# Performance work log

Measured on AMD Instinct MI355X. Metric: run time of the kernel, lower is better.

Reference implementation:

```python
import jax, jax.numpy as jnp
import numpy as np

B, S, F = 64, 1024, 768          # batch, seq = num_patch*patch_size**2, d_model
H, DH = 12, 64                    # heads, head dim = out_dim // d
P2 = 64                           # patch_size ** 2 = attended window length
SCALE = 8.0                       # norm_scale ** 0.5 = (out_dim // d) ** 0.5


def setup_inputs() -> dict:
    key = jax.random.key(0)
    ks = jax.random.split(key, 10)
    std = 0.02
    return {
        "x": jax.random.normal(ks[0], (B, S, F), dtype=jnp.float32),
        # per-head q/k/v projection weights stacked: [H, DH, F] (Linear: y = x @ W.T + b)
        "Wq": jax.random.normal(ks[1], (H, DH, F), dtype=jnp.float32) * std,
        "bq": jax.random.normal(ks[2], (H, DH), dtype=jnp.float32) * std,
        "Wk": jax.random.normal(ks[3], (H, DH, F), dtype=jnp.float32) * std,
        "bk": jax.random.normal(ks[4], (H, DH), dtype=jnp.float32) * std,
        "Wv": jax.random.normal(ks[5], (H, DH, F), dtype=jnp.float32) * std,
        "bv": jax.random.normal(ks[6], (H, DH), dtype=jnp.float32) * std,
        # MHA output projection (only W_MSA[0] is ever used in the stage1 path)
        "Wo": jax.random.normal(ks[7], (F, F), dtype=jnp.float32) * std,
        "bo": jax.random.normal(ks[8], (F,), dtype=jnp.float32) * std,
    }


def reference(x, Wq, bq, Wk, bk, Wv, bv, Wo, bo):
    # stage1 path of SBlock1: only the first window (P2 tokens) goes through
    # MultiHeadAttention (W_MSA[0]); remaining windows are passed through raw
    # and concatenated along the sequence dim.
    xw = x[:, :P2, :]                                    # [B, P2, F]
    q = jnp.einsum('bsf,hdf->bhsd', xw, Wq) + bq[None, :, None, :]
    k = jnp.einsum('bsf,hdf->bhsd', xw, Wk) + bk[None, :, None, :]
    v = jnp.einsum('bsf,hdf->bhsd', xw, Wv) + bv[None, :, None, :]
    scores = jnp.einsum('bhsd,bhtd->bhst', q, k) / SCALE
    attn = jax.nn.softmax(scores, axis=-1)
    o = jnp.einsum('bhst,bhtd->bhsd', attn, v)           # [B, H, P2, DH]
    # heads concatenated along feature dim in order 0..H-1
    o = o.transpose(0, 2, 1, 3).reshape(xw.shape[0], P2, H * DH)
    o = o @ Wo.T + bo                                    # output projection
    return jnp.concatenate([o, x[:, P2:, :]], axis=1)    # [B, S, F]
```

## Files before the change

### kernel.cpp

```cpp
#include <hip/hip_runtime.h>

#define B_   64
#define S_   1024
#define F_   768
#define H_   12
#define DH_  64
#define P2_  64
#define NQKV 2304

using bf16x8 = __attribute__((ext_vector_type(8))) short;
using f32x4  = __attribute__((ext_vector_type(4))) float;

__device__ __forceinline__ unsigned short f2bf(float f) {
    union { float f; unsigned u; } v;
    v.f = f;
    unsigned r = v.u + 0x7FFF + ((v.u >> 16) & 1);
    return (unsigned short)(r >> 16);
}

__device__ __forceinline__ void gll16(const unsigned short* g, unsigned char* l) {
    __builtin_amdgcn_global_load_lds(
        (const __attribute__((address_space(1))) unsigned int*)g,
        (__attribute__((address_space(3))) unsigned int*)l, 16, 0, 0);
}

__global__ __launch_bounds__(256) void prep_kernel(
        const float* __restrict__ x,
        const float* __restrict__ Wq, const float* __restrict__ Wk,
        const float* __restrict__ Wv, const float* __restrict__ Wo,
        const float* __restrict__ bq, const float* __restrict__ bk,
        const float* __restrict__ bv,
        unsigned short* __restrict__ xw, unsigned short* __restrict__ Wqkv,
        unsigned short* __restrict__ Wob, float* __restrict__ bqv) {
    const int NW = 786432;
    const int W4 = 147456;
    int i = blockIdx.x * 256 + threadIdx.x;
    if (i < NW) {
        int b = i / 12288, r = i - b * 12288;
        float4 v = reinterpret_cast<const float4*>(x)[b * 196608 + r];
        ushort4 h;
        h.x = f2bf(v.x); h.y = f2bf(v.y); h.z = f2bf(v.z); h.w = f2bf(v.w);
        reinterpret_cast<ushort4*>(xw)[i] = h;
    } else if (i < NW + 3 * W4) {
        int j = i - NW;
        int which = j / W4, local = j - which * W4;
        const float* src = (which == 0) ? Wq : (which == 1) ? Wk : Wv;
        float4 v = reinterpret_cast<const float4*>(src)[local];
        ushort4 h;
        h.x = f2bf(v.x); h.y = f2bf(v.y); h.z = f2bf(v.z); h.w = f2bf(v.w);
        reinterpret_cast<ushort4*>(Wqkv)[j] = h;
    } else if (i < NW + 4 * W4) {
        int local = i - NW - 3 * W4;
        float4 v = reinterpret_cast<const float4*>(Wo)[local];
        ushort4 h;
        h.x = f2bf(v.x); h.y = f2bf(v.y); h.z = f2bf(v.z); h.w = f2bf(v.w);
        reinterpret_cast<ushort4*>(Wob)[local] = h;
    } else if (i < NW + 4 * W4 + 576) {
        int j4 = i - NW - 4 * W4;
        int seg = j4 / 192, local = j4 - seg * 192;
        const float* src = (seg == 0) ? bq : (seg == 1) ? bk : bv;
        reinterpret_cast<float4*>(bqv)[j4] =
            reinterpret_cast<const float4*>(src)[local];
    }
}

template <int BM, int BN, int OUT_MODE>
__device__ __forceinline__ void gemm_body(
        int bx, int by,
        const unsigned short* __restrict__ A, const unsigned short* __restrict__ Bw,
        const float* __restrict__ bias, void* __restrict__ Cout) {
    constexpr int WC = (BN == 128) ? 2 : 1;
    constexpr int WR = 4 / WC;
    constexpr int MI = BM / WR / 16;
    constexpr int NJ = BN / WC / 16;
    constexpr int CA = BM / 32;
    constexpr int CB = BN / 32;
    __shared__ __align__(16) unsigned char lds[(BM + BN) * 128];
    unsigned char* As = lds;
    unsigned char* Bs = lds + BM * 128;
    const int tid  = threadIdx.x;
    const int lane = tid & 63;
    const int w    = tid >> 6;
    const int wr = w / WC, wc = w % WC;
    const int mbase = wr * (BM / WR), nbase = wc * (BN / WC);
    const int m0 = by * BM, n0 = bx * BN;
    const int lr = lane >> 3, lc = lane & 7;

    f32x4 acc[MI][NJ] = {};

    for (int kt = 0; kt < 768; kt += 64) {
        __syncthreads();
#pragma unroll
        for (int p = 0; p < CA; ++p) {
            int row = (w * CA + p) * 8 + lr;
            gll16(A + (size_t)(m0 + row) * 768 + kt + ((lc ^ (row & 7)) << 3),
                  As + (w * CA + p) * 1024);
        }
#pragma unroll
        for (int p = 0; p < CB; ++p) {
            int row = (w * CB + p) * 8 + lr;
            gll16(Bw + (size_t)(n0 + row) * 768 + kt + ((lc ^ (row & 7)) << 3),
                  Bs + (w * CB + p) * 1024);
        }
        __syncthreads();
#pragma unroll
        for (int kk = 0; kk < 2; ++kk) {
            const int g = kk * 4 + (lane >> 4);
            bf16x8 a[MI], b[NJ];
#pragma unroll
            for (int i = 0; i < MI; ++i) {
                int row = mbase + i * 16 + (lane & 15);
                a[i] = *reinterpret_cast<const bf16x8*>(As + row * 128 + ((g ^ (row & 7)) << 4));
            }
#pragma unroll
            for (int j = 0; j < NJ; ++j) {
                int row = nbase + j * 16 + (lane & 15);
                b[j] = *reinterpret_cast<const bf16x8*>(Bs + row * 128 + ((g ^ (row & 7)) << 4));
            }
#pragma unroll
            for (int i = 0; i < MI; ++i)
#pragma unroll
                for (int j = 0; j < NJ; ++j)
                    acc[i][j] = __builtin_amdgcn_mfma_f32_16x16x32_bf16(a[i], b[j], acc[i][j], 0, 0, 0);
        }
    }

    float bj[NJ];
#pragma unroll
    for (int j = 0; j < NJ; ++j) bj[j] = bias[n0 + nbase + j * 16 + (lane & 15)];

#pragma unroll
    for (int i = 0; i < MI; ++i) {
        int mrow = m0 + mbase + i * 16 + ((lane >> 4) << 2);
#pragma unroll
        for (int j = 0; j < NJ; ++j) {
            int n = n0 + nbase + j * 16 + (lane & 15);
#pragma unroll
            for (int r = 0; r < 4; ++r) {
                float v = acc[i][j][r] + bj[j];
                if constexpr (OUT_MODE == 0) {
                    reinterpret_cast<unsigned short*>(Cout)[(size_t)(mrow + r) * 2304 + n] = f2bf(v);
                } else {
                    int m = mrow + r;
                    reinterpret_cast<float*>(Cout)[(size_t)(m >> 6) * 786432 + (m & 63) * 768 + n] = v;
                }
            }
        }
    }
}

__global__ __launch_bounds__(256) void mega_kernel(
        const float* __restrict__ x, float* __restrict__ out,
        const unsigned short* __restrict__ xw, const unsigned short* __restrict__ Wqkv,
        const float* __restrict__ bqv, unsigned short* __restrict__ Y) {
    if (blockIdx.x < 2048) {
        const int total4 = 11796480;
        int stride = 2048 * 256;
        for (int i = blockIdx.x * 256 + threadIdx.x; i < total4; i += stride) {
            int b = i / 184320, r = i - b * 184320;
            int idx = b * 196608 + 12288 + r;
            reinterpret_cast<float4*>(out)[idx] =
                reinterpret_cast<const float4*>(x)[idx];
        }
    } else {
        int gid = blockIdx.x - 2048;
        gemm_body<128, 128, 0>(gid % 18, gid / 18, xw, Wqkv, bqv, (void*)Y);
    }
}

__global__ __launch_bounds__(256) void oproj_kernel(
        const unsigned short* __restrict__ Obuf, const unsigned short* __restrict__ Wob,
        const float* __restrict__ bo, float* __restrict__ out) {
    gemm_body<64, 64, 1>(blockIdx.x, blockIdx.y, Obuf, Wob, bo, (void*)out);
}

__global__ __launch_bounds__(256) void attn_kernel(
        const unsigned short* __restrict__ Y, unsigned short* __restrict__ O) {
    const int bh = blockIdx.x;
    const int b = bh / 12, h = bh % 12;
    __shared__ __align__(16) unsigned char lds[32768];
    unsigned char* Qs = lds;
    unsigned char* Ks = lds + 8192;
    unsigned char* Vt = lds + 16384;
    unsigned char* Ps = lds + 24576;
    const int tid = threadIdx.x, lane = tid & 63, w = tid >> 6;

    for (int c = tid; c < 512; c += 256) {
        int row = c >> 3, cc = c & 7;
        const unsigned short* src = Y + (size_t)(b * 64 + row) * NQKV + h * 64 + cc * 8;
        *reinterpret_cast<int4*>(Qs + row * 128 + ((cc ^ (row & 7)) << 4)) =
            *reinterpret_cast<const int4*>(src);
        *reinterpret_cast<int4*>(Ks + row * 128 + ((cc ^ (row & 7)) << 4)) =
            *reinterpret_cast<const int4*>(src + 768);
        int4 vv = *reinterpret_cast<const int4*>(src + 1536);
        const unsigned short* vs = reinterpret_cast<const unsigned short*>(&vv);
#pragma unroll
        for (int u = 0; u < 8; ++u) {
            int d = cc * 8 + u;
            *reinterpret_cast<unsigned short*>(
                Vt + d * 128 + (((row >> 3) ^ u) << 4) + ((row & 7) << 1)) = vs[u];
        }
    }
    __syncthreads();

    f32x4 accS[4] = {};
#pragma unroll
    for (int kk = 0; kk < 2; ++kk) {
        const int g = kk * 4 + (lane >> 4);
        int qrow = w * 16 + (lane & 15);
        bf16x8 a = *reinterpret_cast<const bf16x8*>(Qs + qrow * 128 + ((g ^ (qrow & 7)) << 4));
#pragma unroll
        for (int j = 0; j < 4; ++j) {
            int krow = j * 16 + (lane & 15);
            bf16x8 bb = *reinterpret_cast<const bf16x8*>(Ks + krow * 128 + ((g ^ (krow & 7)) << 4));
            accS[j] = __builtin_amdgcn_mfma_f32_16x16x32_bf16(a, bb, accS[j], 0, 0, 0);
        }
    }

#pragma unroll
    for (int r = 0; r < 4; ++r) {
        float v0 = accS[0][r], v1 = accS[1][r], v2 = accS[2][r], v3 = accS[3][r];
        float mx = fmaxf(fmaxf(v0, v1), fmaxf(v2, v3));
        mx = fmaxf(mx, __shfl_xor(mx, 1));
        mx = fmaxf(mx, __shfl_xor(mx, 2));
        mx = fmaxf(mx, __shfl_xor(mx, 4));
        mx = fmaxf(mx, __shfl_xor(mx, 8));
        float p0 = __expf((v0 - mx) * 0.125f);
        float p1 = __expf((v1 - mx) * 0.125f);
        float p2 = __expf((v2 - mx) * 0.125f);
        float p3 = __expf((v3 - mx) * 0.125f);
        float sm = p0 + p1 + p2 + p3;
        sm += __shfl_xor(sm, 1);
        sm += __shfl_xor(sm, 2);
        sm += __shfl_xor(sm, 4);
        sm += __shfl_xor(sm, 8);
        float inv = 1.0f / sm;
        int srow = w * 16 + ((lane >> 4) << 2) + r;
        float pv[4] = {p0 * inv, p1 * inv, p2 * inv, p3 * inv};
#pragma unroll
        for (int j = 0; j < 4; ++j) {
            int t = j * 16 + (lane & 15);
            *reinterpret_cast<unsigned short*>(
                Ps + srow * 128 + (((t >> 3) ^ (srow & 7)) << 4) + ((t & 7) << 1)) = f2bf(pv[j]);
        }
    }
    __syncthreads();

    f32x4 accO[4] = {};
#pragma unroll
    for (int kk = 0; kk < 2; ++kk) {
        const int g = kk * 4 + (lane >> 4);
        int prow = w * 16 + (lane & 15);
        bf16x8 a = *reinterpret_cast<const bf16x8*>(Ps + prow * 128 + ((g ^ (prow & 7)) << 4));
#pragma unroll
        for (int j = 0; j < 4; ++j) {
            int drow = j * 16 + (lane & 15);
            bf16x8 bb = *reinterpret_cast<const bf16x8*>(Vt + drow * 128 + ((g ^ (drow & 7)) << 4));
            accO[j] = __builtin_amdgcn_mfma_f32_16x16x32_bf16(a, bb, accO[j], 0, 0, 0);
        }
    }

#pragma unroll
    for (int j = 0; j < 4; ++j) {
        int d = h * 64 + j * 16 + (lane & 15);
#pragma unroll
        for (int r = 0; r < 4; ++r) {
            int s = w * 16 + ((lane >> 4) << 2) + r;
            O[(size_t)(b * 64 + s) * 768 + d] = f2bf(accO[j][r]);
        }
    }
}

extern "C" void kernel_launch(void* const* d_in, const int* in_sizes, int n_in,
                              void* d_out, int out_size, void* d_ws, size_t ws_size,
                              hipStream_t stream) {
    const float* x  = (const float*)d_in[0];
    const float* Wq = (const float*)d_in[1];
    const float* bq = (const float*)d_in[2];
    const float* Wk = (const float*)d_in[3];
    const float* bk = (const float*)d_in[4];
    const float* Wv = (const float*)d_in[5];
    const float* bv = (const float*)d_in[6];
    const float* Wo = (const float*)d_in[7];
    const float* bo = (const float*)d_in[8];
    float* out = (float*)d_out;
    char* ws = (char*)d_ws;

    unsigned short* xw   = (unsigned short*)(ws);
    unsigned short* Wqkv = (unsigned short*)(ws + 6291456);
    unsigned short* Wob  = (unsigned short*)(ws + 9830400);
    float*          bqv  = (float*)(ws + 11010048);
    unsigned short* Y    = (unsigned short*)(ws + 11019264);
    unsigned short* Obuf = (unsigned short*)(ws + 29893632);

    prep_kernel<<<5379, 256, 0, stream>>>(x, Wq, Wk, Wv, Wo, bq, bk, bv,
                                          xw, Wqkv, Wob, bqv);
    mega_kernel<<<2624, 256, 0, stream>>>(x, out, xw, Wqkv, bqv, Y);
    attn_kernel<<<768, 256, 0, stream>>>(Y, Obuf);
    oproj_kernel<<<dim3(12, 64), 256, 0, stream>>>(Obuf, Wob, bo, out);
}
```

Baseline: 414.0 us.

## Split passthrough copy across QKV, attention, and output-projection kernels

The passthrough copy of the non-attended windows (x[:,64:,:] to out) previously ran entirely in the QKV-GEMM mega kernel. It is now split into three chunks run by extra blocks in the QKV GEMM, attention, and output-projection kernels, so the bandwidth-bound copy overlaps with the compute-bound stages. GEMM blocks are also placed first in the grid so they get scheduled early. The risk is that copy blocks compete with GEMM or attention blocks for bandwidth and CU slots.

Measured after the change: 400.7 us. -3.2%, faster.

```diff
diff --git a/kernel.cpp b/kernel.cpp
--- a/kernel.cpp
+++ b/kernel.cpp
@@ -22,6 +22,19 @@
     __builtin_amdgcn_global_load_lds(
         (const __attribute__((address_space(1))) unsigned int*)g,
         (__attribute__((address_space(3))) unsigned int*)l, 16, 0, 0);
+}
+
+__device__ __forceinline__ void copy_role(const float* __restrict__ x,
+                                          float* __restrict__ out,
+                                          int off4, int cnt4, int nblk, int bid) {
+    int stride = nblk * 256;
+    for (int i = bid * 256 + threadIdx.x; i < cnt4; i += stride) {
+        int j = off4 + i;
+        int b = j / 184320, r = j - b * 184320;
+        int idx = b * 196608 + 12288 + r;
+        reinterpret_cast<float4*>(out)[idx] =
+            reinterpret_cast<const float4*>(x)[idx];
+    }
 }
 
 __global__ __launch_bounds__(256) void prep_kernel(
@@ -153,29 +166,31 @@
         const float* __restrict__ x, float* __restrict__ out,
         const unsigned short* __restrict__ xw, const unsigned short* __restrict__ Wqkv,
         const float* __restrict__ bqv, unsigned short* __restrict__ Y) {
-    if (blockIdx.x < 2048) {
-        const int total4 = 11796480;
-        int stride = 2048 * 256;
-        for (int i = blockIdx.x * 256 + threadIdx.x; i < total4; i += stride) {
-            int b = i / 184320, r = i - b * 184320;
-            int idx = b * 196608 + 12288 + r;
-            reinterpret_cast<float4*>(out)[idx] =
-                reinterpret_cast<const float4*>(x)[idx];
-        }
+    if (blockIdx.x < 576) {
+        gemm_body<128, 128, 0>(blockIdx.x % 18, blockIdx.x / 18, xw, Wqkv, bqv, (void*)Y);
     } else {
-        int gid = blockIdx.x - 2048;
-        gemm_body<128, 128, 0>(gid % 18, gid / 18, xw, Wqkv, bqv, (void*)Y);
+        copy_role(x, out, 0, 7077888, 1536, blockIdx.x - 576);
     }
 }
 
 __global__ __launch_bounds__(256) void oproj_kernel(
         const unsigned short* __restrict__ Obuf, const unsigned short* __restrict__ Wob,
-        const float* __restrict__ bo, float* __restrict__ out) {
-    gemm_body<64, 64, 1>(blockIdx.x, blockIdx.y, Obuf, Wob, bo, (void*)out);
+        const float* __restrict__ bo, float* __restrict__ out,
+        const float* __restrict__ x) {
+    if (blockIdx.x < 768) {
+        gemm_body<64, 64, 1>(blockIdx.x % 12, blockIdx.x / 12, Obuf, Wob, bo, (void*)out);
+    } else {
+        copy_role(x, out, 8257536, 3538944, 1024, blockIdx.x - 768);
+    }
 }
 
 __global__ __launch_bounds__(256) void attn_kernel(
-        const unsigned short* __restrict__ Y, unsigned short* __restrict__ O) {
+        const unsigned short* __restrict__ Y, unsigned short* __restrict__ O,
+        const float* __restrict__ x, float* __restrict__ out) {
+    if (blockIdx.x >= 768) {
+        copy_role(x, out, 7077888, 1179648, 512, blockIdx.x - 768);
+        return;
+    }
     const int bh = blockIdx.x;
     const int b = bh / 12, h = bh % 12;
     __shared__ __align__(16) unsigned char lds[32768];
@@ -295,7 +310,7 @@
 
     prep_kernel<<<5379, 256, 0, stream>>>(x, Wq, Wk, Wv, Wo, bq, bk, bv,
                                           xw, Wqkv, Wob, bqv);
-    mega_kernel<<<2624, 256, 0, stream>>>(x, out, xw, Wqkv, bqv, Y);
-    attn_kernel<<<768, 256, 0, stream>>>(Y, Obuf);
-    oproj_kernel<<<dim3(12, 64), 256, 0, stream>>>(Obuf, Wob, bo, out);
-}
+    mega_kernel<<<2112, 256, 0, stream>>>(x, out, xw, Wqkv, bqv, Y);
+    attn_kernel<<<1280, 256, 0, stream>>>(Y, Obuf, x, out);
+    oproj_kernel<<<1792, 256, 0, stream>>>(Obuf, Wob, bo, out, x);
+}
```
